# Performance work log

Measured on AMD Instinct MI355X. Metric: run time of the kernel, lower is better.

## Reference

```python
import jax, jax.numpy as jnp
import numpy as np

B_, S_, F_, N_, H_ = 4, 8192, 512, 64, 2048  # batch, seq, features, state_dim, mlp hidden
EPS = 1e-5


def setup_inputs() -> dict:
    key = jax.random.key(0)
    ks = jax.random.split(key, 24)
    F, N, H = F_, N_, H_

    def nrm(k, shape, scale=1.0):
        return jax.random.normal(k, shape, dtype=jnp.float32) * scale

    inp = {}
    inp['x'] = nrm(ks[0], (B_, S_, F))
    inp['cond'] = nrm(ks[1], (B_, F))
    n = jnp.arange(N, dtype=jnp.float32)
    for i, p in enumerate(['fwd', 'bwd']):
        b = 2 + i * 6
        inp[p + '_logAre'] = jnp.log(n + 0.5)          # HiPPO-diag: A_real = -(n+0.5)
        inp[p + '_Aim'] = jnp.pi * n                    # HiPPO-diag: A_imag = pi*n
        inp[p + '_Bre'] = nrm(ks[b], (N, F), 1.0 / np.sqrt(N))
        inp[p + '_Bim'] = nrm(ks[b + 1], (N, F), 1.0 / np.sqrt(N))
        inp[p + '_Cre'] = nrm(ks[b + 2], (F, N), 1.0 / np.sqrt(F))
        inp[p + '_Cim'] = nrm(ks[b + 3], (F, N), 1.0 / np.sqrt(F))
        inp[p + '_D'] = nrm(ks[b + 4], (F,))
        inp[p + '_logdt'] = jax.random.uniform(ks[b + 5], (N,), minval=jnp.log(0.001), maxval=jnp.log(0.1))
    inp['proj_w'] = nrm(ks[14], (2 * F, F), 1.0 / np.sqrt(2 * F))
    inp['proj_b'] = jnp.zeros((F,), jnp.float32)
    # AdaLN modulation: Dense(6F) on silu(cond); zero-init in the model, small random here
    inp['ada_w'] = nrm(ks[15], (F, 6 * F), 0.02)
    inp['ada_b'] = jnp.zeros((6 * F,), jnp.float32)
    inp['mlp_w1'] = nrm(ks[16], (F, H), 1.0 / np.sqrt(F))
    inp['mlp_b1'] = jnp.zeros((H,), jnp.float32)
    inp['mlp_w2'] = nrm(ks[17], (H, F), 1.0 / np.sqrt(H))
    inp['mlp_b2'] = jnp.zeros((F,), jnp.float32)
    return inp


def _ln(x):
    mu = jnp.mean(x, axis=-1, keepdims=True)
    v = jnp.mean(jnp.square(x - mu), axis=-1, keepdims=True)
    return (x - mu) * jax.lax.rsqrt(v + EPS)


def _s5(u, logAre, Aim, Bre, Bim, Cre, Cim, D, logdt):
    dt = jnp.exp(logdt)
    A = -jnp.exp(logAre) + 1j * Aim                       # [N] complex diagonal
    A_bar = jnp.exp(A * dt)                               # ZOH discretization
    B_bar = (A_bar[:, None] - 1.0) / (A[:, None] + 1e-8) * (Bre + 1j * Bim)  # [N,F]
    u32 = u.astype(jnp.float32)
    Bu = jnp.einsum('bsf,nf->bsn', u32, B_bar)            # [B,S,N] complex
    Ab = jnp.broadcast_to(A_bar[None, None, :], Bu.shape)

    def op(e1, e2):
        a1, b1 = e1
        a2, b2 = e2
        return (a1 * a2, a2 * b1 + b2)

    _, xs = jax.lax.associative_scan(op, (Ab, Bu), axis=1)
    y = jnp.einsum('fn,bsn->bsf', Cre + 1j * Cim, xs).real + D * u32
    return y.astype(u.dtype)


def reference(x, cond, fwd_logAre, fwd_Aim, fwd_Bre, fwd_Bim, fwd_Cre, fwd_Cim, fwd_D, fwd_logdt,
              bwd_logAre, bwd_Aim, bwd_Bre, bwd_Bim, bwd_Cre, bwd_Cim, bwd_D, bwd_logdt,
              proj_w, proj_b, ada_w, ada_b, mlp_w1, mlp_b1, mlp_w2, mlp_b2):
    mods = jax.nn.silu(cond) @ ada_w + ada_b              # [B,6F]
    sh1, sc1, g1, sh2, sc2, g2 = [m[:, None, :] for m in jnp.split(mods, 6, axis=-1)]
    h = _ln(x) * (1.0 + sc1) + sh1
    y_fwd = _s5(h, fwd_logAre, fwd_Aim, fwd_Bre, fwd_Bim, fwd_Cre, fwd_Cim, fwd_D, fwd_logdt)
    y_bwd = jnp.flip(_s5(jnp.flip(h, axis=1), bwd_logAre, bwd_Aim, bwd_Bre, bwd_Bim, bwd_Cre, bwd_Cim, bwd_D, bwd_logdt), axis=1)
    y = jnp.concatenate([y_fwd, y_bwd], axis=-1) @ proj_w + proj_b
    x = x + g1 * y
    h2 = _ln(x) * (1.0 + sc2) + sh2
    x = x + g2 * (jax.nn.gelu(h2 @ mlp_w1 + mlp_b1) @ mlp_w2 + mlp_b2)
    return x
```

## Files before the change

### kernel.cpp

```cpp
#include <hip/hip_runtime.h>
#include <hip/hip_bf16.h>

typedef unsigned short u16;
typedef __attribute__((ext_vector_type(8))) short bf16x8;
typedef __attribute__((ext_vector_type(4))) float f32x4;

#define Bc 4
#define Sc 8192
#define Fc 512
#define Nc 64
#define Hc 2048
#define Tc 32768
#define SIXF 3072

__device__ __forceinline__ u16 f2bf(float v) {
  __hip_bfloat16 h = __float2bfloat16(v);
  return *reinterpret_cast<u16*>(&h);
}
__device__ __forceinline__ float bf2f(u16 u) {
  return __uint_as_float(((unsigned)u) << 16);
}
__device__ __forceinline__ float ldf(const void* p, long i, int bf) {
  return bf ? bf2f(((const u16*)p)[i]) : ((const float*)p)[i];
}

__device__ __forceinline__ void ld16(const u16* g, u16* l) {
  __builtin_amdgcn_global_load_lds(
      (const __attribute__((address_space(1))) unsigned int*)g,
      (__attribute__((address_space(3))) unsigned int*)l,
      16, 0, 0);
}

__device__ __forceinline__ void xcd_swz(int& bx, int& by) {
  int gx = gridDim.x;
  int nwg = gx * gridDim.y;
  int lin = blockIdx.x + gx * blockIdx.y;
  if ((nwg & 7) == 0) {
    int q = nwg >> 3;
    lin = (lin & 7) * q + (lin >> 3);
  }
  bx = lin % gx;
  by = lin / gx;
}

__global__ void k_detect(const u16* __restrict__ x, int* __restrict__ flag) {
  if (threadIdx.x == 0) {
    int cnt = 0;
    for (int i = 0; i < 256; ++i) {
      int e = (x[i] >> 7) & 0xFF;
      cnt += (e >= 130);
    }
    *flag = (cnt >= 16) ? 0 : 1;
  }
}

__global__ void k_convert(const void* __restrict__ src, float* __restrict__ dst,
                          int n, const int* __restrict__ flag) {
  int bf = *flag;
  int i = blockIdx.x * blockDim.x + threadIdx.x;
  int stride = gridDim.x * blockDim.x;
  for (int j = i; j < n; j += stride) dst[j] = ldf(src, j, bf);
}

__global__ __launch_bounds__(256) void k_mods_init(const void* __restrict__ ada_b,
                                                   const int* __restrict__ flag,
                                                   float* __restrict__ mods) {
  int bf = *flag;
  int col = blockIdx.x * 256 + threadIdx.x;
  float v = ldf(ada_b, col, bf);
  for (int b = 0; b < Bc; ++b) mods[b * SIXF + col] = v;
}

__global__ __launch_bounds__(256) void k_mods2(const void* __restrict__ cond,
                                               const void* __restrict__ ada_w,
                                               const int* __restrict__ flag,
                                               float* __restrict__ mods) {
  int bf = *flag;
  int b = blockIdx.y;
  int f0 = blockIdx.z * 128;
  int col = blockIdx.x * 256 + threadIdx.x;
  __shared__ float sc[128];
  for (int i = threadIdx.x; i < 128; i += 256) {
    float c = ldf(cond, b * Fc + f0 + i, bf);
    sc[i] = c / (1.f + expf(-c));
  }
  __syncthreads();
  float acc = 0.f;
  for (int f = 0; f < 128; ++f) acc = fmaf(sc[f], ldf(ada_w, (long)(f0 + f) * SIXF + col, bf), acc);
  atomicAdd(&mods[b * SIXF + col], acc);
}

__global__ void k_prep(const void* lAf, const void* Aif, const void* Brf, const void* Bif, const void* ldtf,
                       const void* lAb, const void* Aib, const void* Brb, const void* Bib, const void* ldtb,
                       const int* __restrict__ flag,
                       u16* __restrict__ Wbup, float* __restrict__ Abar) {
  int bf = *flag;
  int dir = blockIdx.x;
  int f0 = blockIdx.y * 64;
  int n = threadIdx.x;
  const void* lA = dir ? lAb : lAf;
  const void* Ai = dir ? Aib : Aif;
  const void* Br = dir ? Brb : Brf;
  const void* Bi = dir ? Bib : Bif;
  const void* ld = dir ? ldtb : ldtf;
  float dt  = expf(ldf(ld, n, bf));
  float Are = -expf(ldf(lA, n, bf));
  float Aim = ldf(Ai, n, bf);
  float er  = expf(Are * dt);
  float abr = er * cosf(Aim * dt);
  float abi = er * sinf(Aim * dt);
  if (blockIdx.y == 0) {
    Abar[(dir * Nc + n) * 2 + 0] = abr;
    Abar[(dir * Nc + n) * 2 + 1] = abi;
  }
  float dr = Are + 1e-8f, di = Aim;
  float den = dr * dr + di * di;
  float nr = abr - 1.f, ni = abi;
  float cr = (nr * dr + ni * di) / den;
  float ci = (ni * dr - nr * di) / den;
  int col_re = dir * 128 + n, col_im = dir * 128 + 64 + n;
  for (int f = f0; f < f0 + 64; ++f) {
    float br = ldf(Br, n * Fc + f, bf), bi = ldf(Bi, n * Fc + f, bf);
    Wbup[(((f >> 3) * 256) + col_re) * 8 + (f & 7)] = f2bf(cr * br - ci * bi);
    Wbup[(((f >> 3) * 256) + col_im) * 8 + (f & 7)] = f2bf(cr * bi + ci * br);
  }
}

__global__ __launch_bounds__(256) void k_P2p(const void* Df, const void* Db, const void* pw,
                                             const int* __restrict__ flag, u16* __restrict__ P2p) {
  int bf = *flag;
  int idx = blockIdx.x * 256 + threadIdx.x;
  int f1 = idx >> 9, fo = idx & 511;
  float v = ldf(Df, f1, bf) * ldf(pw, (long)f1 * Fc + fo, bf) +
            ldf(Db, f1, bf) * ldf(pw, (long)(Fc + f1) * Fc + fo, bf);
  P2p[(((f1 >> 3) * Fc) + fo) * 8 + (f1 & 7)] = f2bf(v);
}

__global__ __launch_bounds__(256) void k_Cpm(const void* Cref, const void* Cimf,
                                             const void* Creb, const void* Cimb,
                                             const int* __restrict__ flag, u16* __restrict__ Cpm) {
  int bf = *flag;
  int k = blockIdx.x;
  int dir = k >> 7, c = (k >> 6) & 1, n = k & 63;
  const void* C = dir ? (c ? Cimb : Creb) : (c ? Cimf : Cref);
  float sgn = c ? -1.f : 1.f;
  for (int f = threadIdx.x; f < Fc; f += 256)
    Cpm[k * Fc + f] = f2bf(sgn * ldf(C, (long)f * Nc + n, bf));
}

__global__ __launch_bounds__(256) void k_Wpack(const void* __restrict__ src, const int* __restrict__ flag,
                                               int log2N, u16* __restrict__ dst) {
  int bf = *flag;
  long i = (long)blockIdx.x * 256 + threadIdx.x;
  int Nn = 1 << log2N;
  long k8 = i >> log2N;
  int n = (int)(i & (Nn - 1));
  u16 tmp[8];
#pragma unroll
  for (int j = 0; j < 8; ++j)
    tmp[j] = f2bf(ldf(src, ((k8 << 3) + j) * (long)Nn + n, bf));
  *(ushort4*)(dst + i * 8)     = *(ushort4*)tmp;
  *(ushort4*)(dst + i * 8 + 4) = *(ushort4*)(tmp + 4);
}

__global__ __launch_bounds__(256) void k_ln(const void* __restrict__ src, int srcmode,
                                            long src_tok_base, int b0,
                                            const int* __restrict__ flag,
                                            const float* __restrict__ mods,
                                            int sh_base, int sc_base,
                                            u16* __restrict__ dst) {
  int bf = srcmode ? 1 : *flag;
  long lt = blockIdx.x;
  int b = b0 + (int)(lt >> 13);
  int t = threadIdx.x;
  long si = (src_tok_base + lt) * Fc;
  float x0 = ldf(src, si + t, bf);
  float x1 = ldf(src, si + t + 256, bf);
  float s = x0 + x1, qq = x0 * x0 + x1 * x1;
  for (int o = 32; o; o >>= 1) { s += __shfl_down(s, o); qq += __shfl_down(qq, o); }
  __shared__ float ss[4], sq[4];
  int w = t >> 6;
  if ((t & 63) == 0) { ss[w] = s; sq[w] = qq; }
  __syncthreads();
  float S = ss[0] + ss[1] + ss[2] + ss[3];
  float Q = sq[0] + sq[1] + sq[2] + sq[3];
  float mu = S * (1.f / Fc);
  float var = Q * (1.f / Fc) - mu * mu;
  float rs = rsqrtf(var + 1e-5f);
  const float* mb = mods + b * SIXF;
  float h0 = (x0 - mu) * rs * (1.f + mb[sc_base + t]) + mb[sh_base + t];
  float h1 = (x1 - mu) * rs * (1.f + mb[sc_base + t + 256]) + mb[sh_base + t + 256];
  dst[lt * Fc + t] = f2bf(h0);
  dst[lt * Fc + t + 256] = f2bf(h1);
}

struct Smem { u16 As[128 * 64]; u16 Ws[64 * 128]; };

__device__ __forceinline__ void mfma_gemm(Smem& sm, const u16* __restrict__ A, long row0, int K,
                                          const u16* __restrict__ Wp, int N, int col0,
                                          f32x4 (&acc)[4][4]) {
  const int tid = threadIdx.x;
  const int l = tid & 63;
  const int q = l >> 4, li = l & 15;
  const int w = tid >> 6;
  const int wm = (w >> 1) << 6, wn = (w & 1) << 6;
  const int m0 = tid >> 3;
  const int kc0 = (tid & 7) ^ (m0 & 7);
  const long aoff0 = (row0 + m0) * (long)K + (kc0 << 3);
  const long woff0 = (long)(tid >> 7) * ((long)N << 3) + ((long)(col0 + (tid & 127)) << 3);
  u16* asdst = sm.As + ((w << 6) << 3);
  u16* wsdst = sm.Ws + ((w << 6) << 3);
  for (int k0 = 0; k0 < K; k0 += 64) {
    __syncthreads();
#pragma unroll
    for (int it = 0; it < 4; ++it)
      ld16(A + aoff0 + (long)it * ((long)K << 5) + k0, asdst + (it << 11));
#pragma unroll
    for (int it = 0; it < 4; ++it)
      ld16(Wp + woff0 + (long)k0 * N + (long)it * ((long)N << 4), wsdst + (it << 11));
    __syncthreads();
#pragma unroll
    for (int ks = 0; ks < 2; ++ks) {
      bf16x8 af[4], bw[4];
#pragma unroll
      for (int mt = 0; mt < 4; ++mt) {
        int mrow = wm + (mt << 4) + li;
        af[mt] = *(const bf16x8*)(sm.As + (((mrow << 3) + (((ks << 2) + q) ^ (mrow & 7))) << 3));
      }
#pragma unroll
      for (int nt = 0; nt < 4; ++nt) {
        int n = wn + (nt << 4) + li;
        bw[nt] = *(const bf16x8*)(sm.Ws + ((((((ks << 2) + q) << 7) + n)) << 3));
      }
#pragma unroll
      for (int mt = 0; mt < 4; ++mt)
#pragma unroll
        for (int nt = 0; nt < 4; ++nt)
          acc[mt][nt] = __builtin_amdgcn_mfma_f32_16x16x32_bf16(af[mt], bw[nt], acc[mt][nt], 0, 0, 0);
    }
  }
}

__global__ __launch_bounds__(256) void k_Gp2(const u16* __restrict__ Cpm, const u16* __restrict__ pwp,
                                             u16* __restrict__ Gp) {
  __shared__ Smem sm;
  f32x4 acc[4][4] = {};
  int bx, by; xcd_swz(bx, by);
  long row0 = (long)by * 128;
  int col0 = bx << 7;
  int dir = (int)(row0 >> 7);
  mfma_gemm(sm, Cpm, row0, Fc, pwp + (size_t)dir * 262144, Fc, col0, acc);
  const int l = threadIdx.x & 63, q = l >> 4, li = l & 15;
  const int w = threadIdx.x >> 6;
  const int wm = (w >> 1) << 6, wn = (w & 1) << 6;
#pragma unroll
  for (int mt = 0; mt < 4; ++mt)
#pragma unroll
    for (int nt = 0; nt < 4; ++nt)
#pragma unroll
      for (int r = 0; r < 4; ++r) {
        int k = (int)row0 + wm + (mt << 4) + (q << 2) + r;
        int col = col0 + wn + (nt << 4) + li;
        Gp[(((k >> 3) * Fc) + col) * 8 + (k & 7)] = f2bf(acc[mt][nt][r]);
      }
}

__global__ __launch_bounds__(256) void k_gemm_bu(const u16* __restrict__ h,
                                                 const u16* __restrict__ Wbup,
                                                 int nb, float* __restrict__ Bu) {
  __shared__ Smem sm;
  f32x4 acc[4][4] = {};
  int bx, by; xcd_swz(bx, by);
  long row0 = (long)by * 128;
  int col0 = bx << 7;
  mfma_gemm(sm, h, row0, Fc, Wbup, 256, col0, acc);
  const int l = threadIdx.x & 63, q = l >> 4, li = l & 15;
  const int w = threadIdx.x >> 6;
  const int wm = (w >> 1) << 6, wn = (w & 1) << 6;
#pragma unroll
  for (int mt = 0; mt < 4; ++mt) {
#pragma unroll
    for (int nt = 0; nt < 4; ++nt) {
      int col = col0 + wn + (nt << 4) + li;
      int dir = col >> 7, cc = (col >> 6) & 1, n = col & 63;
#pragma unroll
      for (int r = 0; r < 4; ++r) {
        long lt = row0 + wm + (mt << 4) + (q << 2) + r;
        int lb = (int)(lt >> 13), s = (int)(lt & 8191);
        int spos = dir ? (Sc - 1 - s) : s;
        Bu[((((long)dir * nb + lb) * Nc + n) * Sc + spos) * 2 + cc] = acc[mt][nt][r];
      }
    }
  }
}

__global__ __launch_bounds__(256) void k_scan(float* __restrict__ Bu, const float* __restrict__ Abar,
                                              int nb) {
  int blk = blockIdx.x;
  int per_dir = nb * 64;
  int dir = blk / per_dir;
  int rem = blk - dir * per_dir;
  int lb = rem >> 6, n = rem & 63;
  float ar = Abar[(dir * Nc + n) * 2 + 0];
  float ai = Abar[(dir * Nc + n) * 2 + 1];
  float* base = Bu + (((long)dir * nb + lb) * Nc + n) * Sc * 2;
  int t = threadIdx.x;
  float4 loc[16];
  float lr = 0.f, li = 0.f;
  const float4* bp = (const float4*)base + t * 16;
#pragma unroll
  for (int j = 0; j < 16; ++j) {
    float4 v = bp[j];
    loc[j] = v;
    float nr = fmaf(ar, lr, fmaf(-ai, li, v.x));
    float ni = fmaf(ar, li, fmaf(ai, lr, v.y));
    lr = fmaf(ar, nr, fmaf(-ai, ni, v.z));
    li = fmaf(ar, ni, fmaf(ai, nr, v.w));
  }
  __shared__ float sr[256], si[256];
  float pr = ar, pi = ai;
  for (int k = 0; k < 5; ++k) { float t2 = pr * pr - pi * pi; pi = 2.f * pr * pi; pr = t2; }
  float vr = lr, vi = li;
  for (int step = 1; step < 256; step <<= 1) {
    sr[t] = vr; si[t] = vi;
    __syncthreads();
    if (t >= step) {
      float orr = sr[t - step], oii = si[t - step];
      vr = vr + pr * orr - pi * oii;
      vi = vi + pr * oii + pi * orr;
    }
    __syncthreads();
    float t2 = pr * pr - pi * pi; pi = 2.f * pr * pi; pr = t2;
  }
  sr[t] = vr; si[t] = vi;
  __syncthreads();
  float xr = (t == 0) ? 0.f : sr[t - 1];
  float xi = (t == 0) ? 0.f : si[t - 1];
  float4* op = (float4*)base + t * 16;
#pragma unroll
  for (int j = 0; j < 16; ++j) {
    float4 v = loc[j];
    float nr = fmaf(ar, xr, fmaf(-ai, xi, v.x));
    float ni = fmaf(ar, xi, fmaf(ai, xr, v.y));
    xr = fmaf(ar, nr, fmaf(-ai, ni, v.z));
    xi = fmaf(ar, ni, fmaf(ai, nr, v.w));
    float4 o; o.x = nr; o.y = ni; o.z = xr; o.w = xi;
    op[j] = o;
  }
}

__global__ __launch_bounds__(256) void k_xs_t(const float* __restrict__ xs, int nb,
                                              u16* __restrict__ xh, u16* __restrict__ xl) {
  __shared__ float tile[32 * 257];
  long t0 = (long)blockIdx.x * 32;
  int lb = (int)(t0 >> 13);
  int s0 = (int)(t0 & 8191);
  int tid = threadIdx.x;
  int ls = tid & 31;
  int half = (tid >> 5) & 1;
  int wv = tid >> 6;
#pragma unroll 4
  for (int cg = 0; cg < 32; ++cg) {
    int col = cg * 8 + wv * 2 + half;
    int dir = col >> 7, cc = (col >> 6) & 1, n = col & 63;
    int spos = dir ? (Sc - 1 - (s0 + ls)) : (s0 + ls);
    float v = xs[((((long)dir * nb + lb) * Nc + n) * Sc + spos) * 2 + cc];
    tile[ls * 257 + col] = v;
  }
  __syncthreads();
  for (int j = 0; j < 32; ++j) {
    float v = tile[j * 257 + tid];
    u16 hi = f2bf(v);
    long lt = t0 + j;
    xh[lt * 256 + tid] = hi;
    xl[lt * 256 + tid] = f2bf(v - bf2f(hi));
  }
}

__global__ __launch_bounds__(256) void k_gemm_y(const u16* __restrict__ xh, const u16* __restrict__ xl,
                                                const u16* __restrict__ Gp,
                                                const u16* __restrict__ h, const u16* __restrict__ P2p,
                                                const void* __restrict__ xraw, long tok_base, int b0,
                                                const int* __restrict__ flag,
                                                const float* __restrict__ mods, const float* __restrict__ pb,
                                                u16* __restrict__ out1) {
  __shared__ Smem sm;
  f32x4 acc[4][4] = {};
  int bx, by; xcd_swz(bx, by);
  long row0 = (long)by * 128;
  int col0 = bx << 7;
  mfma_gemm(sm, xh, row0, 256, Gp, Fc, col0, acc);
  mfma_gemm(sm, xl, row0, 256, Gp, Fc, col0, acc);
  mfma_gemm(sm, h, row0, Fc, P2p, Fc, col0, acc);
  int bf = *flag;
  const int l = threadIdx.x & 63, q = l >> 4, li = l & 15;
  const int w = threadIdx.x >> 6;
  const int wm = (w >> 1) << 6, wn = (w & 1) << 6;
#pragma unroll
  for (int mt = 0; mt < 4; ++mt) {
#pragma unroll
    for (int r = 0; r < 4; ++r) {
      long lt = row0 + wm + (mt << 4) + (q << 2) + r;
      int b = b0 + (int)(lt >> 13);
      const float* mb = mods + b * SIXF + 2 * Fc;
#pragma unroll
      for (int nt = 0; nt < 4; ++nt) {
        int col = col0 + wn + (nt << 4) + li;
        float xv = ldf(xraw, (tok_base + lt) * Fc + col, bf);
        out1[lt * Fc + col] = f2bf(xv + mb[col] * (acc[mt][nt][r] + pb[col]));
      }
    }
  }
}

__device__ __forceinline__ float gelu_t(float u) {
  float z = 0.7978845608028654f * fmaf(0.044715f * u * u, u, u);
  float e = __builtin_amdgcn_exp2f(z * -2.8853900817779268f);
  return u * __builtin_amdgcn_rcpf(1.f + e);
}

__global__ __launch_bounds__(256) void k_mlp1(const u16* __restrict__ h2, const u16* __restrict__ W1p,
                                              const float* __restrict__ b1, long crow0,
                                              u16* __restrict__ tbuf) {
  __shared__ Smem sm;
  f32x4 acc[4][4] = {};
  int bx, by; xcd_swz(bx, by);
  long row0 = crow0 + (long)by * 128;
  int col0 = bx << 7;
  mfma_gemm(sm, h2, row0, Fc, W1p, Hc, col0, acc);
  const int l = threadIdx.x & 63, q = l >> 4, li = l & 15;
  const int w = threadIdx.x >> 6;
  const int wm = (w >> 1) << 6, wn = (w & 1) << 6;
#pragma unroll
  for (int mt = 0; mt < 4; ++mt) {
#pragma unroll
    for (int r = 0; r < 4; ++r) {
      long lr2 = row0 - crow0 + wm + (mt << 4) + (q << 2) + r;
#pragma unroll
      for (int nt = 0; nt < 4; ++nt) {
        int col = col0 + wn + (nt << 4) + li;
        tbuf[lr2 * Hc + col] = f2bf(gelu_t(acc[mt][nt][r] + b1[col]));
      }
    }
  }
}

__global__ __launch_bounds__(256) void k_mlp2(const u16* __restrict__ tbuf, const u16* __restrict__ W2p,
                                              const float* __restrict__ b2, const u16* __restrict__ out1,
                                              const float* __restrict__ mods, long crow0,
                                              long tok_base, int b0,
                                              const int* __restrict__ flag, void* __restrict__ dout) {
  __shared__ Smem sm;
  f32x4 acc[4][4] = {};
  int bx, by; xcd_swz(bx, by);
  long lrow0 = (long)by * 128;
  int col0 = bx << 7;
  mfma_gemm(sm, tbuf, lrow0, Hc, W2p, Fc, col0, acc);
  int bf = *flag;
  const int l = threadIdx.x & 63, q = l >> 4, li = l & 15;
  const int w = threadIdx.x >> 6;
  const int wm = (w >> 1) << 6, wn = (w & 1) << 6;
#pragma unroll
  for (int mt = 0; mt < 4; ++mt) {
#pragma unroll
    for (int r = 0; r < 4; ++r) {
      long lt = crow0 + lrow0 + wm + (mt << 4) + (q << 2) + r;
      int b = b0 + (int)(lt >> 13);
      const float* mb = mods + b * SIXF + 5 * Fc;
#pragma unroll
      for (int nt = 0; nt < 4; ++nt) {
        int col = col0 + wn + (nt << 4) + li;
        float v = bf2f(out1[lt * Fc + col]) + mb[col] * (acc[mt][nt][r] + b2[col]);
        long oi = (tok_base + lt) * Fc + col;
        if (bf) ((u16*)dout)[oi] = f2bf(v);
        else    ((float*)dout)[oi] = v;
      }
    }
  }
}

extern "C" void kernel_launch(void* const* d_in, const int* in_sizes, int n_in,
                              void* d_out, int out_size, void* d_ws, size_t ws_size,
                              hipStream_t stream) {
  char* ws = (char*)d_ws;
  size_t off = 0;
  auto alloc = [&](size_t bytes) -> char* {
    char* p = ws + off;
    off += (bytes + 255) & ~(size_t)255;
    return p;
  };
  int*   flag = (int*)  alloc(4);
  float* mods = (float*)alloc((size_t)Bc * SIXF * 4);
  float* Abar = (float*)alloc(2 * Nc * 2 * 4);
  float* pbf  = (float*)alloc(Fc * 4);
  float* b1f  = (float*)alloc(Hc * 4);
  float* b2f  = (float*)alloc(Fc * 4);
  u16* Wbup = (u16*)alloc((size_t)Fc * 256 * 2);
  u16* Gp   = (u16*)alloc((size_t)256 * Fc * 2);
  u16* P2p  = (u16*)alloc((size_t)Fc * Fc * 2);
  u16* W1p  = (u16*)alloc((size_t)Fc * Hc * 2);
  u16* W2p  = (u16*)alloc((size_t)Hc * Fc * 2);
  u16* pwp  = (u16*)alloc((size_t)1024 * Fc * 2);
  u16* Cpm  = (u16*)alloc((size_t)256 * Fc * 2);
  size_t off_static = off;

  const size_t U = (size_t)Sc * Fc * 2;
  int nb = 4;
  while (nb > 1 && off_static + (size_t)nb * 4 * U + 4096 > ws_size) nb >>= 1;

  u16*   h    = (u16*)  alloc((size_t)nb * U);
  float* Bu   = (float*)alloc((size_t)nb * U);
  u16*   xh   = (u16*)  alloc((size_t)nb * U / 2);
  u16*   xl   = (u16*)  alloc((size_t)nb * U / 2);
  u16*   out1 = (u16*)  alloc((size_t)nb * U);
  u16* tch = (u16*)Bu;
  u16* h2  = h;

  k_detect<<<1, 64, 0, stream>>>((const u16*)d_in[0], flag);
  k_convert<<<2, 256, 0, stream>>>(d_in[19], pbf, Fc, flag);
  k_convert<<<8, 256, 0, stream>>>(d_in[23], b1f, Hc, flag);
  k_convert<<<2, 256, 0, stream>>>(d_in[25], b2f, Fc, flag);
  k_mods_init<<<12, 256, 0, stream>>>(d_in[21], flag, mods);
  k_mods2<<<dim3(12, Bc, 4), 256, 0, stream>>>(d_in[1], d_in[20], flag, mods);
  k_prep<<<dim3(2, 8), 64, 0, stream>>>(d_in[2], d_in[3], d_in[4], d_in[5], d_in[9],
                                        d_in[10], d_in[11], d_in[12], d_in[13], d_in[17],
                                        flag, Wbup, Abar);
  k_P2p<<<(Fc * Fc) / 256, 256, 0, stream>>>(d_in[8], d_in[16], d_in[18], flag, P2p);
  k_Wpack<<<256, 256, 0, stream>>>(d_in[18], flag, 9, pwp);
  k_Cpm<<<256, 256, 0, stream>>>(d_in[6], d_in[7], d_in[14], d_in[15], flag, Cpm);
  k_Gp2<<<dim3(4, 2), 256, 0, stream>>>(Cpm, pwp, Gp);
  k_Wpack<<<512, 256, 0, stream>>>(d_in[22], flag, 11, W1p);
  k_Wpack<<<512, 256, 0, stream>>>(d_in[24], flag, 9, W2p);

  for (int b0 = 0; b0 < Bc; b0 += nb) {
    long tok_base = (long)b0 * Sc;
    long rows = (long)nb * Sc;
    k_ln<<<rows, 256, 0, stream>>>(d_in[0], 0, tok_base, b0, flag, mods, 0, Fc, h);
    k_gemm_bu<<<dim3(2, rows / 128), 256, 0, stream>>>(h, Wbup, nb, Bu);
    k_scan<<<2 * nb * 64, 256, 0, stream>>>(Bu, Abar, nb);
    k_xs_t<<<rows / 32, 256, 0, stream>>>(Bu, nb, xh, xl);
    k_gemm_y<<<dim3(Fc / 128, rows / 128), 256, 0, stream>>>(xh, xl, Gp, h, P2p,
                                                             d_in[0], tok_base, b0, flag, mods, pbf, out1);
    k_ln<<<rows, 256, 0, stream>>>(out1, 1, 0, b0, flag, mods, 3 * Fc, 4 * Fc, h2);
    long RC = rows / 2;
    for (int ch = 0; ch < 2; ++ch) {
      long crow0 = ch * RC;
      k_mlp1<<<dim3(Hc / 128, RC / 128), 256, 0, stream>>>(h2, W1p, b1f, crow0, tch);
      k_mlp2<<<dim3(Fc / 128, RC / 128), 256, 0, stream>>>(tch, W2p, b2f, out1, mods, crow0,
                                                           tok_base, b0, flag, d_out);
    }
  }
  (void)n_in; (void)out_size; (void)in_sizes;
}
```

Before: 667.8 us.

## Double-buffer LDS tiles in shared MFMA GEMM to overlap loads with compute

The shared GEMM routine now keeps two LDS buffers for the A and W tiles. It issues the global-to-LDS loads for the next K-step before running the MFMAs on the current one, and needs only one barrier per step instead of two. The active buffer index is threaded through consecutive GEMM calls in k_gemm_y, so chained accumulations keep alternating buffers safely. The cost is double the LDS per block, which can reduce how many blocks fit on a CU at once.

```diff
diff --git a/kernel.cpp b/kernel.cpp
--- a/kernel.cpp
+++ b/kernel.cpp
@@ -194,11 +194,12 @@
   dst[lt * Fc + t + 256] = f2bf(h1);
 }
 
-struct Smem { u16 As[128 * 64]; u16 Ws[64 * 128]; };
-
-__device__ __forceinline__ void mfma_gemm(Smem& sm, const u16* __restrict__ A, long row0, int K,
-                                          const u16* __restrict__ Wp, int N, int col0,
-                                          f32x4 (&acc)[4][4]) {
+struct Smem { u16 As[2][128 * 64]; u16 Ws[2][64 * 128]; };
+
+__device__ __forceinline__ int mfma_gemm(Smem& sm, int cur,
+                                         const u16* __restrict__ A, long row0, int K,
+                                         const u16* __restrict__ Wp, int N, int col0,
+                                         f32x4 (&acc)[4][4]) {
   const int tid = threadIdx.x;
   const int l = tid & 63;
   const int q = l >> 4, li = l & 15;
@@ -208,29 +209,39 @@
   const int kc0 = (tid & 7) ^ (m0 & 7);
   const long aoff0 = (row0 + m0) * (long)K + (kc0 << 3);
   const long woff0 = (long)(tid >> 7) * ((long)N << 3) + ((long)(col0 + (tid & 127)) << 3);
-  u16* asdst = sm.As + ((w << 6) << 3);
-  u16* wsdst = sm.Ws + ((w << 6) << 3);
-  for (int k0 = 0; k0 < K; k0 += 64) {
-    __syncthreads();
+  const int lbase = w << 9;
+  const int T = K >> 6;
+
+  auto stage = [&](int buf, int k0) {
 #pragma unroll
     for (int it = 0; it < 4; ++it)
-      ld16(A + aoff0 + (long)it * ((long)K << 5) + k0, asdst + (it << 11));
+      ld16(A + aoff0 + (long)it * ((long)K << 5) + k0, sm.As[buf] + lbase + (it << 11));
 #pragma unroll
     for (int it = 0; it < 4; ++it)
-      ld16(Wp + woff0 + (long)k0 * N + (long)it * ((long)N << 4), wsdst + (it << 11));
-    __syncthreads();
+      ld16(Wp + woff0 + (long)k0 * N + (long)it * ((long)N << 4), sm.Ws[buf] + lbase + (it << 11));
+  };
+
+  stage(cur, 0);
+  asm volatile("s_waitcnt vmcnt(0)" ::: "memory");
+  __builtin_amdgcn_s_barrier();
+  __builtin_amdgcn_sched_barrier(0);
+
+  for (int t = 0; t < T; ++t) {
+    if (t + 1 < T) stage(cur ^ 1, (t + 1) << 6);
+    const u16* As = sm.As[cur];
+    const u16* Ws = sm.Ws[cur];
 #pragma unroll
     for (int ks = 0; ks < 2; ++ks) {
       bf16x8 af[4], bw[4];
 #pragma unroll
       for (int mt = 0; mt < 4; ++mt) {
         int mrow = wm + (mt << 4) + li;
-        af[mt] = *(const bf16x8*)(sm.As + (((mrow << 3) + (((ks << 2) + q) ^ (mrow & 7))) << 3));
+        af[mt] = *(const bf16x8*)(As + (((mrow << 3) + (((ks << 2) + q) ^ (mrow & 7))) << 3));
       }
 #pragma unroll
       for (int nt = 0; nt < 4; ++nt) {
         int n = wn + (nt << 4) + li;
-        bw[nt] = *(const bf16x8*)(sm.Ws + ((((((ks << 2) + q) << 7) + n)) << 3));
+        bw[nt] = *(const bf16x8*)(Ws + ((((((ks << 2) + q) << 7) + n)) << 3));
       }
 #pragma unroll
       for (int mt = 0; mt < 4; ++mt)
@@ -238,7 +249,14 @@
         for (int nt = 0; nt < 4; ++nt)
           acc[mt][nt] = __builtin_amdgcn_mfma_f32_16x16x32_bf16(af[mt], bw[nt], acc[mt][nt], 0, 0, 0);
     }
-  }
+    if (t + 1 < T) {
+      asm volatile("s_waitcnt vmcnt(0)" ::: "memory");
+      __builtin_amdgcn_s_barrier();
+      __builtin_amdgcn_sched_barrier(0);
+    }
+    cur ^= 1;
+  }
+  return cur;
 }
 
 __global__ __launch_bounds__(256) void k_Gp2(const u16* __restrict__ Cpm, const u16* __restrict__ pwp,
@@ -249,7 +267,7 @@
   long row0 = (long)by * 128;
   int col0 = bx << 7;
   int dir = (int)(row0 >> 7);
-  mfma_gemm(sm, Cpm, row0, Fc, pwp + (size_t)dir * 262144, Fc, col0, acc);
+  mfma_gemm(sm, 0, Cpm, row0, Fc, pwp + (size_t)dir * 262144, Fc, col0, acc);
   const int l = threadIdx.x & 63, q = l >> 4, li = l & 15;
   const int w = threadIdx.x >> 6;
   const int wm = (w >> 1) << 6, wn = (w & 1) << 6;
@@ -273,7 +291,7 @@
   int bx, by; xcd_swz(bx, by);
   long row0 = (long)by * 128;
   int col0 = bx << 7;
-  mfma_gemm(sm, h, row0, Fc, Wbup, 256, col0, acc);
+  mfma_gemm(sm, 0, h, row0, Fc, Wbup, 256, col0, acc);
   const int l = threadIdx.x & 63, q = l >> 4, li = l & 15;
   const int w = threadIdx.x >> 6;
   const int wm = (w >> 1) << 6, wn = (w & 1) << 6;
@@ -389,9 +407,10 @@
   int bx, by; xcd_swz(bx, by);
   long row0 = (long)by * 128;
   int col0 = bx << 7;
-  mfma_gemm(sm, xh, row0, 256, Gp, Fc, col0, acc);
-  mfma_gemm(sm, xl, row0, 256, Gp, Fc, col0, acc);
-  mfma_gemm(sm, h, row0, Fc, P2p, Fc, col0, acc);
+  int cur = 0;
+  cur = mfma_gemm(sm, cur, xh, row0, 256, Gp, Fc, col0, acc);
+  cur = mfma_gemm(sm, cur, xl, row0, 256, Gp, Fc, col0, acc);
+  cur = mfma_gemm(sm, cur, h, row0, Fc, P2p, Fc, col0, acc);
   int bf = *flag;
   const int l = threadIdx.x & 63, q = l >> 4, li = l & 15;
   const int w = threadIdx.x >> 6;
@@ -427,7 +446,7 @@
   int bx, by; xcd_swz(bx, by);
   long row0 = crow0 + (long)by * 128;
   int col0 = bx << 7;
-  mfma_gemm(sm, h2, row0, Fc, W1p, Hc, col0, acc);
+  mfma_gemm(sm, 0, h2, row0, Fc, W1p, Hc, col0, acc);
   const int l = threadIdx.x & 63, q = l >> 4, li = l & 15;
   const int w = threadIdx.x >> 6;
   const int wm = (w >> 1) << 6, wn = (w & 1) << 6;
@@ -455,7 +474,7 @@
   int bx, by; xcd_swz(bx, by);
   long lrow0 = (long)by * 128;
   int col0 = bx << 7;
-  mfma_gemm(sm, tbuf, lrow0, Hc, W2p, Fc, col0, acc);
+  mfma_gemm(sm, 0, tbuf, lrow0, Hc, W2p, Fc, col0, acc);
   int bf = *flag;
   const int l = threadIdx.x & 63, q = l >> 4, li = l & 15;
   const int w = threadIdx.x >> 6;
```

Result: faster. 639.5 us (-4.3%).
